# Performance work log

Measured on AMD Instinct MI355X. Metric: run time of the kernel, lower is better.

Reference implementation:

```python
import jax, jax.numpy as jnp
import numpy as np

NUM_HEADS = 16
HEAD_DIM = 80
HIDDEN = 1280
SEQ = 3072
NUM_SEGS = 6  # 6 packed images of 512 patches each


def rotate_half(x):
    x1, x2 = jnp.split(x, 2, axis=-1)
    return jnp.concatenate([-x2, x1], axis=-1)


def setup_inputs() -> dict:
    key = jax.random.key(0)
    ks = jax.random.split(key, 6)
    hidden_states = jax.random.normal(ks[0], (SEQ, HIDDEN), dtype=jnp.float32)
    # RoPE tables as in Qwen-VL vision: freqs over half the head_dim, duplicated
    half = HEAD_DIM // 2
    inv_freq = 1.0 / (10000.0 ** (jnp.arange(half, dtype=jnp.float32) / half))
    pos = jnp.arange(SEQ, dtype=jnp.float32)[:, None]
    freqs = pos * inv_freq[None, :]                      # (SEQ, half)
    emb = jnp.concatenate([freqs, freqs], axis=-1)       # (SEQ, HEAD_DIM)
    cos = jnp.cos(emb)
    sin = jnp.sin(emb)
    # Packed segment boundaries: [0, 512, 1024, ..., 3072]
    cu_seqlens = jnp.arange(0, SEQ + 1, SEQ // NUM_SEGS, dtype=jnp.int32)
    scale = 0.02
    w_qkv = jax.random.normal(ks[1], (3 * HIDDEN, HIDDEN), dtype=jnp.float32) * scale
    b_qkv = jax.random.normal(ks[2], (3 * HIDDEN,), dtype=jnp.float32) * scale
    w_proj = jax.random.normal(ks[3], (HIDDEN, HIDDEN), dtype=jnp.float32) * scale
    b_proj = jax.random.normal(ks[4], (HIDDEN,), dtype=jnp.float32) * scale
    return {
        "hidden_states": hidden_states, "cos": cos, "sin": sin,
        "w_qkv": w_qkv, "b_qkv": b_qkv, "w_proj": w_proj, "b_proj": b_proj,
        "cu_seqlens": cu_seqlens,
    }


def reference(hidden_states, cos, sin, w_qkv, b_qkv, w_proj, b_proj, cu_seqlens):
    S, H = hidden_states.shape
    nh, hd = NUM_HEADS, H // NUM_HEADS

    # Fused QKV projection: (S, 3H) -> q, k, v each (S, nh, hd)
    qkv = hidden_states @ w_qkv.T + b_qkv
    qkv = qkv.reshape(S, 3, nh, hd)
    q, k, v = qkv[:, 0], qkv[:, 1], qkv[:, 2]

    # Inline RoPE on q/k (cos/sin broadcast over heads)
    c = cos[:, None, :]
    s = sin[:, None, :]
    q = q * c + rotate_half(q) * s
    k = k * c + rotate_half(k) * s

    # Original casts fp32 -> fp16 for the flash attention kernel
    q16 = q.astype(jnp.float16)
    k16 = k.astype(jnp.float16)
    v16 = v.astype(jnp.float16)

    # Varlen masking: tokens attend only within their own packed segment
    tok = jnp.arange(S)
    seg = jnp.searchsorted(cu_seqlens, tok, side="right")  # (S,)
    same_seg = seg[:, None] == seg[None, :]                 # (S, S)

    scale = hd ** (-0.5)
    # Scores accumulated in fp32 (as flash attention does internally)
    scores = jnp.einsum("qhd,khd->hqk", q16, k16,
                        preferred_element_type=jnp.float32) * scale
    scores = jnp.where(same_seg[None], scores, jnp.finfo(jnp.float32).min)
    weights = jax.nn.softmax(scores, axis=-1).astype(jnp.float16)  # (nh, S, S)

    attn = jnp.einsum("hqk,khd->qhd", weights, v16)  # (S, nh, hd) fp16
    attn = attn.astype(jnp.float32).reshape(S, H)
    return attn @ w_proj.T + b_proj
```

## Files before the change

kernel.cpp:

```cpp
#include <hip/hip_runtime.h>

typedef _Float16 f16;
typedef _Float16 half8 __attribute__((ext_vector_type(8)));
typedef _Float16 half4 __attribute__((ext_vector_type(4)));
typedef float f32x4 __attribute__((ext_vector_type(4)));

__device__ __forceinline__ void gld_lds16(const void* g, void* l) {
  __builtin_amdgcn_global_load_lds((const __attribute__((address_space(1))) void*)g,
                                   (__attribute__((address_space(3))) void*)l, 16, 0, 0);
}

__global__ void cvt_all(const float* __restrict__ hid, const float* __restrict__ wq,
                        const float* __restrict__ wp, f16* __restrict__ hid16,
                        f16* __restrict__ wq16, f16* __restrict__ wp16) {
  int b = blockIdx.x;
  const float* in;
  f16* out;
  int i;
  if (b < 3840) { in = hid; out = hid16; i = b * 256 + threadIdx.x; }
  else if (b < 8640) { in = wq; out = wq16; i = (b - 3840) * 256 + threadIdx.x; }
  else { in = wp; out = wp16; i = (b - 8640) * 256 + threadIdx.x; }
  float4 v = ((const float4*)in)[i];
  half4 o;
  o.x = (f16)v.x; o.y = (f16)v.y; o.z = (f16)v.z; o.w = (f16)v.w;
  ((half4*)out)[i] = o;
}

template <bool OUT_F16>
__global__ __launch_bounds__(256, 2) void gemm_bt(const f16* __restrict__ A,
                                                  const f16* __restrict__ B,
                                                  const float* __restrict__ bias,
                                                  void* __restrict__ Cout,
                                                  int K, int lda, int ldb, int ldc) {
  __shared__ f16 As[128 * 32];
  __shared__ f16 Bs[128 * 32];
  const int tid = threadIdx.x, lane = tid & 63, wave = tid >> 6;
  const int bm = blockIdx.x * 128, bn = blockIdx.y * 128;
  const int wm = (wave & 1) * 64, wn = (wave >> 1) * 64;
  const int lm = lane & 15, kq = (lane >> 4) * 8;
  const int arow = tid >> 2, acol = (tid & 3) * 8;

  const f16* Ab = A + (size_t)(bm + arow) * lda + acol;
  const f16* Bb = B + (size_t)(bn + arow) * ldb + acol;
  f16* AsW = As + wave * 512;
  f16* BsW = Bs + wave * 512;

  f32x4 acc[4][4] = {};
  for (int k0 = 0; k0 < K; k0 += 32) {
    gld_lds16(Ab + k0, AsW);
    gld_lds16(Ab + (size_t)64 * lda + k0, AsW + 2048);
    gld_lds16(Bb + k0, BsW);
    gld_lds16(Bb + (size_t)64 * ldb + k0, BsW + 2048);
    __syncthreads();
    half8 af[4], bf[4];
#pragma unroll
    for (int mt = 0; mt < 4; mt++) af[mt] = *(const half8*)&As[(wm + 16 * mt + lm) * 32 + kq];
#pragma unroll
    for (int nt = 0; nt < 4; nt++) bf[nt] = *(const half8*)&Bs[(wn + 16 * nt + lm) * 32 + kq];
#pragma unroll
    for (int mt = 0; mt < 4; mt++)
#pragma unroll
      for (int nt = 0; nt < 4; nt++)
        acc[mt][nt] = __builtin_amdgcn_mfma_f32_16x16x32_f16(af[mt], bf[nt], acc[mt][nt], 0, 0, 0);
    __syncthreads();
  }
  const int q4 = lane >> 4;
#pragma unroll
  for (int mt = 0; mt < 4; mt++)
#pragma unroll
    for (int nt = 0; nt < 4; nt++)
#pragma unroll
      for (int r = 0; r < 4; r++) {
        int gr = bm + wm + 16 * mt + 4 * q4 + r;
        int gc = bn + wn + 16 * nt + lm;
        float v = acc[mt][nt][r] + bias[gc];
        if (OUT_F16)
          ((f16*)Cout)[(size_t)gr * ldc + gc] = (f16)v;
        else
          ((float*)Cout)[(size_t)gr * ldc + gc] = v;
      }
}

template <bool OUT_F16>
__global__ __launch_bounds__(256, 2) void gemm_bt64(const f16* __restrict__ A,
                                                    const f16* __restrict__ B,
                                                    const float* __restrict__ bias,
                                                    void* __restrict__ Cout,
                                                    int K, int lda, int ldb, int ldc) {
  __shared__ f16 As[64 * 32];
  __shared__ f16 Bs[128 * 32];
  const int tid = threadIdx.x, lane = tid & 63, wave = tid >> 6;
  const int bm = blockIdx.x * 64, bn = blockIdx.y * 128;
  const int wm = (wave & 1) * 32, wn = (wave >> 1) * 64;
  const int lm = lane & 15, kq = (lane >> 4) * 8;
  const int arow = tid >> 2, acol = (tid & 3) * 8;

  const f16* Ab = A + (size_t)(bm + arow) * lda + acol;
  const f16* Bb = B + (size_t)(bn + arow) * ldb + acol;
  f16* AsW = As + wave * 512;
  f16* BsW = Bs + wave * 512;

  f32x4 acc[2][4] = {};
  for (int k0 = 0; k0 < K; k0 += 32) {
    gld_lds16(Ab + k0, AsW);
    gld_lds16(Bb + k0, BsW);
    gld_lds16(Bb + (size_t)64 * ldb + k0, BsW + 2048);
    __syncthreads();
    half8 af[2], bf[4];
#pragma unroll
    for (int mt = 0; mt < 2; mt++) af[mt] = *(const half8*)&As[(wm + 16 * mt + lm) * 32 + kq];
#pragma unroll
    for (int nt = 0; nt < 4; nt++) bf[nt] = *(const half8*)&Bs[(wn + 16 * nt + lm) * 32 + kq];
#pragma unroll
    for (int mt = 0; mt < 2; mt++)
#pragma unroll
      for (int nt = 0; nt < 4; nt++)
        acc[mt][nt] = __builtin_amdgcn_mfma_f32_16x16x32_f16(af[mt], bf[nt], acc[mt][nt], 0, 0, 0);
    __syncthreads();
  }
  const int q4 = lane >> 4;
#pragma unroll
  for (int mt = 0; mt < 2; mt++)
#pragma unroll
    for (int nt = 0; nt < 4; nt++)
#pragma unroll
      for (int r = 0; r < 4; r++) {
        int gr = bm + wm + 16 * mt + 4 * q4 + r;
        int gc = bn + wn + 16 * nt + lm;
        float v = acc[mt][nt][r] + bias[gc];
        if (OUT_F16)
          ((f16*)Cout)[(size_t)gr * ldc + gc] = (f16)v;
        else
          ((float*)Cout)[(size_t)gr * ldc + gc] = v;
      }
}

__global__ void rope_v(f16* __restrict__ qkv, const float* __restrict__ cosb,
                       const float* __restrict__ sinb) {
  int idx = blockIdx.x * 256 + threadIdx.x;
  int c = idx % 5;
  int t = idx / 5;
  int h = t % 16; t /= 16;
  int qk = t & 1;
  int s = t >> 1;
  size_t base = (size_t)s * 3840 + qk * 1280 + h * 80 + c * 8;
  half8 x = *(half8*)&qkv[base];
  half8 y = *(half8*)&qkv[base + 40];
  const float* cp = cosb + s * 80 + c * 8;
  const float* sp = sinb + s * 80 + c * 8;
  half8 ox, oy;
#pragma unroll
  for (int i = 0; i < 8; i++) {
    float cs = cp[i], sn = sp[i];
    float xf = (float)x[i], yf = (float)y[i];
    ox[i] = (f16)(xf * cs - yf * sn);
    oy[i] = (f16)(yf * cs + xf * sn);
  }
  *(half8*)&qkv[base] = ox;
  *(half8*)&qkv[base + 40] = oy;
}

__global__ void transpose_v(const f16* __restrict__ qkv, f16* __restrict__ vt) {
  __shared__ f16 tile[64][72];
  const int bs = blockIdx.x * 64;
  const int bd = blockIdx.y * 64;
  const int r = threadIdx.x >> 2, c = (threadIdx.x & 3) * 16;
  *(uint4*)&tile[r][c] = *(const uint4*)&qkv[(size_t)(bs + r) * 3840 + 2560 + bd + c];
  *(uint4*)&tile[r][c + 8] = *(const uint4*)&qkv[(size_t)(bs + r) * 3840 + 2560 + bd + c + 8];
  __syncthreads();
  f16 tmp[16];
#pragma unroll
  for (int i = 0; i < 16; i++) tmp[i] = tile[c + i][r];
  *(uint4*)&vt[(size_t)(bd + r) * 3072 + bs + c] = *(uint4*)&tmp[0];
  *(uint4*)&vt[(size_t)(bd + r) * 3072 + bs + c + 8] = *(uint4*)&tmp[8];
}

__global__ __launch_bounds__(256, 3) void flash_attn3(const f16* __restrict__ qkv,
                                                      const f16* __restrict__ vt,
                                                      f16* __restrict__ attn) {
  constexpr int KS = 84;
  constexpr int VS = 132;
  __shared__ f16 KP[128 * KS + 16];
  __shared__ f16 Vb[80 * VS + 16];
  const int tid = threadIdx.x, lane = tid & 63, wave = tid >> 6;
  const int lm = lane & 15, q4 = lane >> 4;
  const int h = blockIdx.x, g = blockIdx.z;
  const int qbase = g * 512 + blockIdx.y * 64 + wave * 16;
  f16* P = KP + wave * (16 * VS);
  const half8 hz = {};

  const f16* qrow = qkv + (size_t)(qbase + lm) * 3840 + h * 80;
  half8 qf[3];
  qf[0] = *(const half8*)(qrow + q4 * 8);
  qf[1] = *(const half8*)(qrow + 32 + q4 * 8);
  qf[2] = (q4 < 2) ? *(const half8*)(qrow + 64 + q4 * 8) : hz;

  f32x4 oacc[5] = {};
  float mprev[4] = {-1e30f, -1e30f, -1e30f, -1e30f};
  float lsum[4] = {0.f, 0.f, 0.f, 0.f};
  const float sc = 0.11180339887498949f * 1.4426950408889634f;

  for (int j = 0; j < 4; j++) {
    const int kb = g * 512 + j * 128;
    __syncthreads();
#pragma unroll
    for (int i = 0; i < 5; i++) {
      int task = tid + 256 * i;
      int row = task / 10, ch = task % 10;
      uint4 v = *(const uint4*)&qkv[(size_t)(kb + row) * 3840 + 1280 + h * 80 + ch * 8];
      *(uint4*)&KP[row * KS + ch * 8] = v;
    }
#pragma unroll
    for (int i = 0; i < 5; i++) {
      int task = tid + 256 * i;
      int row = task >> 4, ch = task & 15;
      uint4 v = *(const uint4*)&vt[(size_t)(h * 80 + row) * 3072 + kb + ch * 8];
      *(uint4*)&Vb[row * VS + ch * 8] = v;
    }
    __syncthreads();
    f32x4 sacc[8] = {};
#pragma unroll
    for (int nt = 0; nt < 8; nt++) {
      const f16* kr = &KP[(16 * nt + lm) * KS + q4 * 8];
      half8 b0 = *(const half8*)(kr);
      half8 b1 = *(const half8*)(kr + 32);
      half8 b2 = (q4 < 2) ? *(const half8*)(kr + 64) : hz;
      sacc[nt] = __builtin_amdgcn_mfma_f32_16x16x32_f16(qf[0], b0, sacc[nt], 0, 0, 0);
      sacc[nt] = __builtin_amdgcn_mfma_f32_16x16x32_f16(qf[1], b1, sacc[nt], 0, 0, 0);
      sacc[nt] = __builtin_amdgcn_mfma_f32_16x16x32_f16(qf[2], b2, sacc[nt], 0, 0, 0);
    }
    float mnew[4], alpha[4], rs[4];
#pragma unroll
    for (int r = 0; r < 4; r++) {
      float v = -1e30f;
#pragma unroll
      for (int nt = 0; nt < 8; nt++) v = fmaxf(v, sacc[nt][r]);
      v = fmaxf(v, __shfl_xor(v, 1));
      v = fmaxf(v, __shfl_xor(v, 2));
      v = fmaxf(v, __shfl_xor(v, 4));
      v = fmaxf(v, __shfl_xor(v, 8));
      mnew[r] = fmaxf(mprev[r], v * sc);
      alpha[r] = __builtin_exp2f(mprev[r] - mnew[r]);
      mprev[r] = mnew[r];
      rs[r] = 0.f;
    }
#pragma unroll
    for (int nt = 0; nt < 8; nt++)
#pragma unroll
      for (int r = 0; r < 4; r++) {
        float p = __builtin_exp2f(sacc[nt][r] * sc - mnew[r]);
        sacc[nt][r] = p;
        rs[r] += p;
      }
#pragma unroll
    for (int r = 0; r < 4; r++) {
      float v = rs[r];
      v += __shfl_xor(v, 1);
      v += __shfl_xor(v, 2);
      v += __shfl_xor(v, 4);
      v += __shfl_xor(v, 8);
      lsum[r] = alpha[r] * lsum[r] + v;
#pragma unroll
      for (int nt2 = 0; nt2 < 5; nt2++) oacc[nt2][r] *= alpha[r];
    }
    __syncthreads();
#pragma unroll
    for (int nt = 0; nt < 8; nt++)
#pragma unroll
      for (int r = 0; r < 4; r++)
        P[(4 * q4 + r) * VS + 16 * nt + lm] = (f16)sacc[nt][r];
#pragma unroll
    for (int ks = 0; ks < 4; ks++) {
      half8 ap = *(const half8*)&P[lm * VS + ks * 32 + q4 * 8];
#pragma unroll
      for (int nt2 = 0; nt2 < 5; nt2++) {
        half8 bv = *(const half8*)&Vb[(16 * nt2 + lm) * VS + ks * 32 + q4 * 8];
        oacc[nt2] = __builtin_amdgcn_mfma_f32_16x16x32_f16(ap, bv, oacc[nt2], 0, 0, 0);
      }
    }
  }
#pragma unroll
  for (int r = 0; r < 4; r++) {
    float inv = 1.0f / lsum[r];
    int s = qbase + 4 * q4 + r;
#pragma unroll
    for (int nt2 = 0; nt2 < 5; nt2++)
      attn[(size_t)s * 1280 + h * 80 + 16 * nt2 + lm] = (f16)(oacc[nt2][r] * inv);
  }
}

extern "C" void kernel_launch(void* const* d_in, const int* in_sizes, int n_in,
                              void* d_out, int out_size, void* d_ws, size_t ws_size,
                              hipStream_t stream) {
  const float* hidden = (const float*)d_in[0];
  const float* cosb   = (const float*)d_in[1];
  const float* sinb   = (const float*)d_in[2];
  const float* w_qkv  = (const float*)d_in[3];
  const float* b_qkv  = (const float*)d_in[4];
  const float* w_proj = (const float*)d_in[5];
  const float* b_proj = (const float*)d_in[6];

  char* ws = (char*)d_ws;
  f16* hidden16 = (f16*)(ws + 0);
  f16* wqkv16   = (f16*)(ws + 7864320);
  f16* wproj16  = (f16*)(ws + 17694720);
  f16* qkv16    = (f16*)(ws + 20971520);
  f16* attn16   = (f16*)(ws + 44564480);
  f16* vt16     = hidden16;

  cvt_all<<<10240, 256, 0, stream>>>(hidden, w_qkv, w_proj, hidden16, wqkv16, wproj16);

  gemm_bt<true><<<dim3(24, 30), 256, 0, stream>>>(hidden16, wqkv16, b_qkv, qkv16,
                                                  1280, 1280, 1280, 3840);

  rope_v<<<1920, 256, 0, stream>>>(qkv16, cosb, sinb);
  transpose_v<<<dim3(48, 20), 256, 0, stream>>>(qkv16, vt16);

  flash_attn3<<<dim3(16, 8, 6), 256, 0, stream>>>(qkv16, vt16, attn16);

  gemm_bt64<false><<<dim3(48, 10), 256, 0, stream>>>(attn16, wproj16, b_proj, d_out,
                                                     1280, 1280, 1280, 1280);
}
```

Before: 224.6 us.

## Prefetch K/V tiles into registers, use DPP reductions, merge rope and transpose

The attention kernel now loads the next K/V tile from global memory into registers while the P·V MFMAs of the current tile run, then writes that data to LDS at the start of the next iteration. This hides global-load latency behind compute. Row max and sum reductions use DPP moves instead of shuffles, and K fragments are batched per k-step to expose MFMA ILP. The rope and V-transpose kernels are merged into one launch to save a kernel launch, at the cost of extra registers for prefetch buffers under a 3-block occupancy bound.

Result: no change. 228.3 us (+1.7%).

```diff
diff --git a/kernel.cpp b/kernel.cpp
--- a/kernel.cpp
+++ b/kernel.cpp
@@ -8,6 +8,26 @@
 __device__ __forceinline__ void gld_lds16(const void* g, void* l) {
   __builtin_amdgcn_global_load_lds((const __attribute__((address_space(1))) void*)g,
                                    (__attribute__((address_space(3))) void*)l, 16, 0, 0);
+}
+
+template <int CTRL>
+__device__ __forceinline__ float dppf(float x) {
+  return __builtin_bit_cast(float,
+      __builtin_amdgcn_mov_dpp(__builtin_bit_cast(int, x), CTRL, 0xf, 0xf, true));
+}
+__device__ __forceinline__ float dpp_max16(float v) {
+  v = fmaxf(v, dppf<0xB1>(v));
+  v = fmaxf(v, dppf<0x4E>(v));
+  v = fmaxf(v, dppf<0x128>(v));
+  v = fmaxf(v, dppf<0x140>(v));
+  return v;
+}
+__device__ __forceinline__ float dpp_sum16(float v) {
+  v += dppf<0xB1>(v);
+  v += dppf<0x4E>(v);
+  v += dppf<0x128>(v);
+  v += dppf<0x140>(v);
+  return v;
 }
 
 __global__ void cvt_all(const float* __restrict__ hid, const float* __restrict__ wq,
@@ -135,52 +155,54 @@
       }
 }
 
-__global__ void rope_v(f16* __restrict__ qkv, const float* __restrict__ cosb,
-                       const float* __restrict__ sinb) {
-  int idx = blockIdx.x * 256 + threadIdx.x;
-  int c = idx % 5;
-  int t = idx / 5;
-  int h = t % 16; t /= 16;
-  int qk = t & 1;
-  int s = t >> 1;
-  size_t base = (size_t)s * 3840 + qk * 1280 + h * 80 + c * 8;
-  half8 x = *(half8*)&qkv[base];
-  half8 y = *(half8*)&qkv[base + 40];
-  const float* cp = cosb + s * 80 + c * 8;
-  const float* sp = sinb + s * 80 + c * 8;
-  half8 ox, oy;
-#pragma unroll
-  for (int i = 0; i < 8; i++) {
-    float cs = cp[i], sn = sp[i];
-    float xf = (float)x[i], yf = (float)y[i];
-    ox[i] = (f16)(xf * cs - yf * sn);
-    oy[i] = (f16)(yf * cs + xf * sn);
-  }
-  *(half8*)&qkv[base] = ox;
-  *(half8*)&qkv[base + 40] = oy;
-}
-
-__global__ void transpose_v(const f16* __restrict__ qkv, f16* __restrict__ vt) {
+__global__ void rope_transpose(f16* __restrict__ qkv, const float* __restrict__ cosb,
+                               const float* __restrict__ sinb, f16* __restrict__ vt) {
   __shared__ f16 tile[64][72];
-  const int bs = blockIdx.x * 64;
-  const int bd = blockIdx.y * 64;
-  const int r = threadIdx.x >> 2, c = (threadIdx.x & 3) * 16;
-  *(uint4*)&tile[r][c] = *(const uint4*)&qkv[(size_t)(bs + r) * 3840 + 2560 + bd + c];
-  *(uint4*)&tile[r][c + 8] = *(const uint4*)&qkv[(size_t)(bs + r) * 3840 + 2560 + bd + c + 8];
-  __syncthreads();
-  f16 tmp[16];
-#pragma unroll
-  for (int i = 0; i < 16; i++) tmp[i] = tile[c + i][r];
-  *(uint4*)&vt[(size_t)(bd + r) * 3072 + bs + c] = *(uint4*)&tmp[0];
-  *(uint4*)&vt[(size_t)(bd + r) * 3072 + bs + c + 8] = *(uint4*)&tmp[8];
-}
-
-__global__ __launch_bounds__(256, 3) void flash_attn3(const f16* __restrict__ qkv,
+  const int b = blockIdx.x;
+  if (b < 1920) {
+    int idx = b * 256 + threadIdx.x;
+    int c = idx % 5;
+    int t = idx / 5;
+    int h = t % 16; t /= 16;
+    int qk = t & 1;
+    int s = t >> 1;
+    size_t base = (size_t)s * 3840 + qk * 1280 + h * 80 + c * 8;
+    half8 x = *(half8*)&qkv[base];
+    half8 y = *(half8*)&qkv[base + 40];
+    const float* cp = cosb + s * 80 + c * 8;
+    const float* sp = sinb + s * 80 + c * 8;
+    half8 ox, oy;
+#pragma unroll
+    for (int i = 0; i < 8; i++) {
+      float cs = cp[i], sn = sp[i];
+      float xf = (float)x[i], yf = (float)y[i];
+      ox[i] = (f16)(xf * cs - yf * sn);
+      oy[i] = (f16)(yf * cs + xf * sn);
+    }
+    *(half8*)&qkv[base] = ox;
+    *(half8*)&qkv[base + 40] = oy;
+  } else {
+    const int bb = b - 1920;
+    const int bs = (bb % 48) * 64;
+    const int bd = (bb / 48) * 64;
+    const int r = threadIdx.x >> 2, c = (threadIdx.x & 3) * 16;
+    *(uint4*)&tile[r][c] = *(const uint4*)&qkv[(size_t)(bs + r) * 3840 + 2560 + bd + c];
+    *(uint4*)&tile[r][c + 8] = *(const uint4*)&qkv[(size_t)(bs + r) * 3840 + 2560 + bd + c + 8];
+    __syncthreads();
+    f16 tmp[16];
+#pragma unroll
+    for (int i = 0; i < 16; i++) tmp[i] = tile[c + i][r];
+    *(uint4*)&vt[(size_t)(bd + r) * 3072 + bs + c] = *(uint4*)&tmp[0];
+    *(uint4*)&vt[(size_t)(bd + r) * 3072 + bs + c + 8] = *(uint4*)&tmp[8];
+  }
+}
+
+__global__ __launch_bounds__(256, 3) void flash_attn4(const f16* __restrict__ qkv,
                                                       const f16* __restrict__ vt,
                                                       f16* __restrict__ attn) {
   constexpr int KS = 84;
   constexpr int VS = 132;
-  __shared__ f16 KP[128 * KS + 16];
+  __shared__ f16 KP[128 * KS + 96];
   __shared__ f16 Vb[80 * VS + 16];
   const int tid = threadIdx.x, lane = tid & 63, wave = tid >> 6;
   const int lm = lane & 15, q4 = lane >> 4;
@@ -195,50 +217,59 @@
   qf[1] = *(const half8*)(qrow + 32 + q4 * 8);
   qf[2] = (q4 < 2) ? *(const half8*)(qrow + 64 + q4 * 8) : hz;
 
+  int ko[5], kl[5], vo[5], vl[5];
+#pragma unroll
+  for (int i = 0; i < 5; i++) {
+    int task = tid + 256 * i;
+    int krr = task / 10, kcc = task % 10;
+    ko[i] = krr * 3840 + kcc * 8;
+    kl[i] = krr * KS + kcc * 8;
+    int vrr = task >> 4, vcc = task & 15;
+    vo[i] = vrr * 3072 + vcc * 8;
+    vl[i] = vrr * VS + vcc * 8;
+  }
+  const f16* kseg = qkv + (size_t)g * 512 * 3840 + 1280 + h * 80;
+  const f16* vseg = vt + (size_t)h * 80 * 3072 + g * 512;
+
+  uint4 kpf[5], vpf[5];
+#pragma unroll
+  for (int i = 0; i < 5; i++) kpf[i] = *(const uint4*)(kseg + ko[i]);
+#pragma unroll
+  for (int i = 0; i < 5; i++) vpf[i] = *(const uint4*)(vseg + vo[i]);
+
   f32x4 oacc[5] = {};
   float mprev[4] = {-1e30f, -1e30f, -1e30f, -1e30f};
   float lsum[4] = {0.f, 0.f, 0.f, 0.f};
   const float sc = 0.11180339887498949f * 1.4426950408889634f;
 
   for (int j = 0; j < 4; j++) {
-    const int kb = g * 512 + j * 128;
-    __syncthreads();
-#pragma unroll
-    for (int i = 0; i < 5; i++) {
-      int task = tid + 256 * i;
-      int row = task / 10, ch = task % 10;
-      uint4 v = *(const uint4*)&qkv[(size_t)(kb + row) * 3840 + 1280 + h * 80 + ch * 8];
-      *(uint4*)&KP[row * KS + ch * 8] = v;
-    }
-#pragma unroll
-    for (int i = 0; i < 5; i++) {
-      int task = tid + 256 * i;
-      int row = task >> 4, ch = task & 15;
-      uint4 v = *(const uint4*)&vt[(size_t)(h * 80 + row) * 3072 + kb + ch * 8];
-      *(uint4*)&Vb[row * VS + ch * 8] = v;
-    }
-    __syncthreads();
+    __syncthreads();
+#pragma unroll
+    for (int i = 0; i < 5; i++) *(uint4*)&KP[kl[i]] = kpf[i];
+#pragma unroll
+    for (int i = 0; i < 5; i++) *(uint4*)&Vb[vl[i]] = vpf[i];
+    __syncthreads();
+
     f32x4 sacc[8] = {};
 #pragma unroll
-    for (int nt = 0; nt < 8; nt++) {
-      const f16* kr = &KP[(16 * nt + lm) * KS + q4 * 8];
-      half8 b0 = *(const half8*)(kr);
-      half8 b1 = *(const half8*)(kr + 32);
-      half8 b2 = (q4 < 2) ? *(const half8*)(kr + 64) : hz;
-      sacc[nt] = __builtin_amdgcn_mfma_f32_16x16x32_f16(qf[0], b0, sacc[nt], 0, 0, 0);
-      sacc[nt] = __builtin_amdgcn_mfma_f32_16x16x32_f16(qf[1], b1, sacc[nt], 0, 0, 0);
-      sacc[nt] = __builtin_amdgcn_mfma_f32_16x16x32_f16(qf[2], b2, sacc[nt], 0, 0, 0);
-    }
+    for (int ks = 0; ks < 3; ks++) {
+      half8 bk[8];
+#pragma unroll
+      for (int nt = 0; nt < 8; nt++)
+        bk[nt] = (ks < 2 || q4 < 2)
+                     ? *(const half8*)&KP[(16 * nt + lm) * KS + 32 * ks + q4 * 8]
+                     : hz;
+#pragma unroll
+      for (int nt = 0; nt < 8; nt++)
+        sacc[nt] = __builtin_amdgcn_mfma_f32_16x16x32_f16(qf[ks], bk[nt], sacc[nt], 0, 0, 0);
+    }
+
     float mnew[4], alpha[4], rs[4];
 #pragma unroll
     for (int r = 0; r < 4; r++) {
-      float v = -1e30f;
-#pragma unroll
-      for (int nt = 0; nt < 8; nt++) v = fmaxf(v, sacc[nt][r]);
-      v = fmaxf(v, __shfl_xor(v, 1));
-      v = fmaxf(v, __shfl_xor(v, 2));
-      v = fmaxf(v, __shfl_xor(v, 4));
-      v = fmaxf(v, __shfl_xor(v, 8));
+      float v = fmaxf(fmaxf(fmaxf(sacc[0][r], sacc[1][r]), fmaxf(sacc[2][r], sacc[3][r])),
+                      fmaxf(fmaxf(sacc[4][r], sacc[5][r]), fmaxf(sacc[6][r], sacc[7][r])));
+      v = dpp_max16(v);
       mnew[r] = fmaxf(mprev[r], v * sc);
       alpha[r] = __builtin_exp2f(mprev[r] - mnew[r]);
       mprev[r] = mnew[r];
@@ -254,29 +285,38 @@
       }
 #pragma unroll
     for (int r = 0; r < 4; r++) {
-      float v = rs[r];
-      v += __shfl_xor(v, 1);
-      v += __shfl_xor(v, 2);
-      v += __shfl_xor(v, 4);
-      v += __shfl_xor(v, 8);
+      float v = dpp_sum16(rs[r]);
       lsum[r] = alpha[r] * lsum[r] + v;
 #pragma unroll
       for (int nt2 = 0; nt2 < 5; nt2++) oacc[nt2][r] *= alpha[r];
     }
+
     __syncthreads();
 #pragma unroll
     for (int nt = 0; nt < 8; nt++)
 #pragma unroll
       for (int r = 0; r < 4; r++)
         P[(4 * q4 + r) * VS + 16 * nt + lm] = (f16)sacc[nt][r];
+
+    if (j < 3) {
+      const f16* kn = kseg + (size_t)(j + 1) * (128 * 3840);
+      const f16* vn = vseg + (j + 1) * 128;
+#pragma unroll
+      for (int i = 0; i < 5; i++) kpf[i] = *(const uint4*)(kn + ko[i]);
+#pragma unroll
+      for (int i = 0; i < 5; i++) vpf[i] = *(const uint4*)(vn + vo[i]);
+    }
+
 #pragma unroll
     for (int ks = 0; ks < 4; ks++) {
       half8 ap = *(const half8*)&P[lm * VS + ks * 32 + q4 * 8];
-#pragma unroll
-      for (int nt2 = 0; nt2 < 5; nt2++) {
-        half8 bv = *(const half8*)&Vb[(16 * nt2 + lm) * VS + ks * 32 + q4 * 8];
-        oacc[nt2] = __builtin_amdgcn_mfma_f32_16x16x32_f16(ap, bv, oacc[nt2], 0, 0, 0);
-      }
+      half8 bv[5];
+#pragma unroll
+      for (int nt2 = 0; nt2 < 5; nt2++)
+        bv[nt2] = *(const half8*)&Vb[(16 * nt2 + lm) * VS + ks * 32 + q4 * 8];
+#pragma unroll
+      for (int nt2 = 0; nt2 < 5; nt2++)
+        oacc[nt2] = __builtin_amdgcn_mfma_f32_16x16x32_f16(ap, bv[nt2], oacc[nt2], 0, 0, 0);
     }
   }
 #pragma unroll
@@ -313,10 +353,9 @@
   gemm_bt<true><<<dim3(24, 30), 256, 0, stream>>>(hidden16, wqkv16, b_qkv, qkv16,
                                                   1280, 1280, 1280, 3840);
 
-  rope_v<<<1920, 256, 0, stream>>>(qkv16, cosb, sinb);
-  transpose_v<<<dim3(48, 20), 256, 0, stream>>>(qkv16, vt16);
-
-  flash_attn3<<<dim3(16, 8, 6), 256, 0, stream>>>(qkv16, vt16, attn16);
+  rope_transpose<<<2880, 256, 0, stream>>>(qkv16, cosb, sinb, vt16);
+
+  flash_attn4<<<dim3(16, 8, 6), 256, 0, stream>>>(qkv16, vt16, attn16);
 
   gemm_bt64<false><<<dim3(48, 10), 256, 0, stream>>>(attn16, wproj16, b_proj, d_out,
                                                      1280, 1280, 1280, 1280);
```
